# Optimization experiments

Measured on AMD Instinct MI355X. Metric: run time of the kernel, lower is better.

## Reference

```python
import jax, jax.numpy as jnp
import numpy as np

B, T, D, H, L = 4, 128, 768, 770, 40  # batch, token_num, bert dim, head hidden, n_labels


def setup_inputs() -> dict:
    key = jax.random.key(0)
    ks = jax.random.split(key, 7)
    hidden = jax.random.normal(ks[0], (B, T + 1, D), dtype=jnp.float32)
    pred_spans = jnp.sort(jax.random.randint(ks[1], (B, 2), 0, T), axis=1)
    span_avail = jax.random.randint(ks[2], (T, T), 0, 2).astype(jnp.int32)
    # torch nn.Linear: weight init N(0, 0.02), bias init N(0, 1) (normal_(bias, 0) -> mean=0, std=1)
    W1 = (jax.random.normal(ks[3], (2 * D + 1, H)) * 0.02).astype(jnp.float32)
    b1 = jax.random.normal(ks[4], (H,), dtype=jnp.float32)
    W2 = (jax.random.normal(ks[5], (H, L)) * 0.02).astype(jnp.float32)
    b2 = jax.random.normal(ks[6], (L,), dtype=jnp.float32)
    return {"hidden": hidden, "W1": W1, "b1": b1, "W2": W2, "b2": b2,
            "pred_spans": pred_spans, "span_avail": span_avail, "token_num": T}


def reference(hidden, W1, b1, W2, b2, pred_spans, span_avail, token_num):
    # vecs[i] = hidden[:, i+1, :]  (skip [CLS])
    vecs = hidden[:, 1:token_num + 1, :]                      # [B, T, D]
    Bv, Tv, Dv = vecs.shape
    starts = pred_spans[:, 0][:, None, None]                  # [B,1,1]
    ends = pred_spans[:, 1][:, None, None]
    ii = jnp.arange(Tv)[:, None]                              # [T,1]
    jj = jnp.arange(Tv)[None, :]                              # [1,T]
    # indication: 2 if (i,j) == pred span; 1 if strictly inside span with i<=j; else 0
    is_full = (ii == starts) & (jj == ends)                   # [B,T,T]
    inside = (starts <= ii) & (ii <= jj) & (jj <= ends) & (~is_full)
    ind = (2 * is_full + inside).astype(hidden.dtype)         # [B,T,T]
    fi = jnp.broadcast_to(vecs[:, :, None, :], (Bv, Tv, Tv, Dv))
    fj = jnp.broadcast_to(vecs[:, None, :, :], (Bv, Tv, Tv, Dv))
    feat = jnp.concatenate([fi, fj, ind[..., None]], axis=-1)  # [B,T,T,2D+1]
    h = jax.nn.relu(feat @ W1 + b1)                            # [B,T,T,H]
    out = h @ W2 + b2                                          # [B,T,T,L]
    # unavailable spans contribute a zeros row (original appends `zeros`)
    mask = (span_avail >= 1)[None, :, :, None]
    out = jnp.where(mask, out, jnp.zeros((), out.dtype))
    out = out.reshape(Bv, Tv * Tv, -1)                         # span index c = i*T + j
    return jax.nn.log_softmax(out, axis=1)
```

## Files before the change

### kernel.cpp

```cpp
#include <hip/hip_runtime.h>
#include <math.h>

#define BB 4
#define TT 128
#define DD 768
#define HD 770
#define HP 800
#define LL 40
#define TP1 129

typedef __attribute__((ext_vector_type(8))) short s16x8;
typedef __attribute__((ext_vector_type(4))) float f32x4;

#define P_OFF   0
#define Q_OFF   409600
#define W2F_OFF 819200
#define BF1_OFF 838400
#define ACC_OFF 1440512

__device__ __forceinline__ unsigned pkbf(float a, float b) {
    unsigned ua = __float_as_uint(a);
    unsigned ub = __float_as_uint(b);
    return ((ua + 0x8000u) >> 16) | ((ub + 0x8000u) & 0xffff0000u);
}
__device__ __forceinline__ unsigned rne1(float v) {
    unsigned x = __float_as_uint(v);
    return (x + 0x7fffu + ((x >> 16) & 1u)) >> 16;
}

__global__ __launch_bounds__(256) void kPrep(const float* __restrict__ W1,
                                             const float* __restrict__ W2,
                                             float* __restrict__ Q,
                                             unsigned* __restrict__ W2f,
                                             unsigned* __restrict__ Bf1,
                                             float* __restrict__ accum) {
    const int bx = blockIdx.x;
    const int tid = threadIdx.x;
    if (bx < 19) {
        int u = bx * 256 + tid;
        if (u >= 4800) return;
        int nt = u / 1600;
        int rem = u - nt * 1600;
        int ks = rem >> 6;
        int lane = rem & 63;
        int kbase = ks * 32 + ((lane >> 4) << 3);
        int l = nt * 16 + (lane & 15);
        unsigned pk[4];
        #pragma unroll
        for (int sp = 0; sp < 4; ++sp) {
            unsigned w[2];
            #pragma unroll
            for (int e = 0; e < 2; ++e) {
                int k = kbase + 2 * sp + e;
                float v = (k < HD && l < LL) ? W2[k * LL + l] : 0.0f;
                w[e] = rne1(v);
            }
            pk[sp] = w[0] | (w[1] << 16);
        }
        ((uint4*)W2f)[u] = make_uint4(pk[0], pk[1], pk[2], pk[3]);
    } else if (bx < 607) {
        int u = (bx - 19) * 256 + tid;
        int lane = u & 63;
        int g = u >> 6;
        int ks = g % 24;
        int g2 = g / 24;
        int nt = g2 % 49;
        int half = g2 / 49;
        int kbase = ks * 32 + ((lane >> 4) << 3);
        int h = nt * 16 + (lane & 15);
        int row0 = half * DD + kbase;
        unsigned pk[4];
        #pragma unroll
        for (int sp = 0; sp < 4; ++sp) {
            unsigned w[2];
            #pragma unroll
            for (int e = 0; e < 2; ++e) {
                float v = (h < HD) ? W1[(size_t)(row0 + 2 * sp + e) * HD + h] : 0.0f;
                w[e] = rne1(v);
            }
            pk[sp] = w[0] | (w[1] << 16);
        }
        ((uint4*)Bf1)[u] = make_uint4(pk[0], pk[1], pk[2], pk[3]);
    } else {
        int u = (bx - 607) * 256 + tid;
        if (u < 160) accum[u] = 0.0f;
        int u2 = u - 160;
        if (u2 >= 0 && u2 < 512 * 30) {
            int row = u2 / 30;
            int h = HD + (u2 - row * 30);
            Q[(size_t)row * HP + h] = 0.0f;
        }
    }
}

__global__ __launch_bounds__(256) void kA(const float* __restrict__ hidden,
                                          const unsigned* __restrict__ Bf1,
                                          const float* __restrict__ b1,
                                          float* __restrict__ P,
                                          float* __restrict__ Q) {
    __shared__ float part[2 * 64 * 8];
    const int tid  = threadIdx.x;
    const int wave = tid >> 6;
    const int lane = tid & 63;
    const int pairl = wave >> 1;
    const int kh    = wave & 1;
    const int pair  = blockIdx.x * 2 + pairl;
    const int mband = pair & 31;
    const int nt    = pair >> 5;
    const int b  = mband >> 3;
    const int tt = mband & 7;
    const int col  = lane & 15;
    const int quad = lane >> 4;

    const float* __restrict__ Arow =
        hidden + (size_t)(b * TP1 + 1 + tt * 16 + col) * DD + (quad << 3);
    const uint4* __restrict__ B0 = (const uint4*)Bf1 + ((size_t)nt * 24) * 64 + lane;
    const uint4* __restrict__ B1 = (const uint4*)Bf1 + ((size_t)(49 + nt) * 24) * 64 + lane;

    f32x4 a0 = (f32x4){0.f, 0.f, 0.f, 0.f};
    f32x4 a1 = (f32x4){0.f, 0.f, 0.f, 0.f};

    const int ks0 = kh * 12;
    #pragma unroll 4
    for (int s = 0; s < 12; ++s) {
        const int ks = ks0 + s;
        float4 x0 = *(const float4*)(Arow + ks * 32);
        float4 x1 = *(const float4*)(Arow + ks * 32 + 4);
        union { unsigned u[4]; s16x8 v; } af;
        af.u[0] = pkbf(x0.x, x0.y); af.u[1] = pkbf(x0.z, x0.w);
        af.u[2] = pkbf(x1.x, x1.y); af.u[3] = pkbf(x1.z, x1.w);
        union { uint4 q; s16x8 v; } bf0, bf1;
        bf0.q = B0[ks * 64];
        bf1.q = B1[ks * 64];
        a0 = __builtin_amdgcn_mfma_f32_16x16x32_bf16(af.v, bf0.v, a0, 0, 0, 0);
        a1 = __builtin_amdgcn_mfma_f32_16x16x32_bf16(af.v, bf1.v, a1, 0, 0, 0);
    }

    if (kh == 1) {
        float* dst = part + (pairl * 64 + lane) * 8;
        dst[0] = a0[0]; dst[1] = a0[1]; dst[2] = a0[2]; dst[3] = a0[3];
        dst[4] = a1[0]; dst[5] = a1[1]; dst[6] = a1[2]; dst[7] = a1[3];
    }
    __syncthreads();
    if (kh == 0) {
        const float* src = part + (pairl * 64 + lane) * 8;
        const int h = nt * 16 + col;
        if (h < HD) {
            const float bv = b1[h];
            #pragma unroll
            for (int r = 0; r < 4; ++r) {
                int t = tt * 16 + quad * 4 + r;
                size_t row = (size_t)(b * TT + t) * HP;
                P[row + h] = a0[r] + src[r] + bv;
                Q[row + h] = a1[r] + src[4 + r];
            }
        }
    }
}

__global__ __launch_bounds__(256) void kB(const float* __restrict__ P,
                                          const float* __restrict__ Q,
                                          const float* __restrict__ W1,
                                          const unsigned* __restrict__ W2f,
                                          const float* __restrict__ b2,
                                          const int* __restrict__ spans,
                                          const int* __restrict__ avail,
                                          float* __restrict__ out,
                                          float* __restrict__ accum) {
    __shared__ unsigned Sb[2][128 * 20];
    __shared__ float var[3 * HP];
    __shared__ int avi[TT];
    __shared__ float sred[192];

    const int i = blockIdx.x;
    const int b = blockIdx.y;
    const int tid = threadIdx.x;
    const int wave = tid >> 6;
    const int lane = tid & 63;

    const int start = spans[b * 2];
    const int end   = spans[b * 2 + 1];

    const int jS = tid >> 1;
    const int hh = (tid & 1) << 4;
    int indS;
    {
        bool isfull = (i == start) && (jS == end);
        bool inside = (start <= i) && (i <= jS) && (jS <= end) && !isfull;
        indS = isfull ? 2 : (inside ? 1 : 0);
    }

    {
        const float* Pi  = P + (size_t)(b * TT + i) * HP;
        const float* w1L = W1 + (size_t)2 * DD * HD;
        for (int h = tid; h < HP; h += 256) {
            float pv = (h < HD) ? Pi[h] : 0.0f;
            float wv = (h < HD) ? w1L[h] : 0.0f;
            var[h]        = pv;
            var[HP + h]   = pv + wv;
            var[2*HP + h] = pv + wv + wv;
        }
        if (tid < TT) avi[tid] = avail[i * TT + tid];
    }
    __syncthreads();

    const float* Qj = Q + (size_t)(b * TT + jS) * HP;
    const float* vb = var + indS * HP;

    auto form = [&](int c, int p) {
        const int h0 = c * 32 + hh;
        const float4* qp = (const float4*)(Qj + h0);
        float4 q0 = qp[0], q1 = qp[1], q2 = qp[2], q3 = qp[3];
        const float4* vp = (const float4*)(vb + h0);
        float4 v0 = vp[0], v1 = vp[1], v2 = vp[2], v3 = vp[3];
        float s0 = fmaxf(v0.x + q0.x, 0.f), s1 = fmaxf(v0.y + q0.y, 0.f);
        float s2 = fmaxf(v0.z + q0.z, 0.f), s3 = fmaxf(v0.w + q0.w, 0.f);
        float s4 = fmaxf(v1.x + q1.x, 0.f), s5 = fmaxf(v1.y + q1.y, 0.f);
        float s6 = fmaxf(v1.z + q1.z, 0.f), s7 = fmaxf(v1.w + q1.w, 0.f);
        float s8 = fmaxf(v2.x + q2.x, 0.f), s9 = fmaxf(v2.y + q2.y, 0.f);
        float sa = fmaxf(v2.z + q2.z, 0.f), sb_ = fmaxf(v2.w + q2.w, 0.f);
        float sc = fmaxf(v3.x + q3.x, 0.f), sd = fmaxf(v3.y + q3.y, 0.f);
        float se = fmaxf(v3.z + q3.z, 0.f), sf = fmaxf(v3.w + q3.w, 0.f);
        uint4* dst = (uint4*)(&Sb[p][jS * 20 + (hh >> 1)]);
        dst[0] = make_uint4(pkbf(s0,s1), pkbf(s2,s3), pkbf(s4,s5), pkbf(s6,s7));
        dst[1] = make_uint4(pkbf(s8,s9), pkbf(sa,sb_), pkbf(sc,sd), pkbf(se,sf));
    };

    f32x4 acc[2][3];
    #pragma unroll
    for (int mt = 0; mt < 2; ++mt)
        #pragma unroll
        for (int nt = 0; nt < 3; ++nt)
            acc[mt][nt] = (f32x4){0.f, 0.f, 0.f, 0.f};

    form(0, 0);
    __syncthreads();

    const int arow0 = (wave * 32 + (lane & 15)) * 20 + ((lane >> 4) << 2);
    for (int c = 0; c < 25; ++c) {
        const int p = c & 1;
        s16x8 bf0 = *(const s16x8*)((const unsigned*)W2f + (( 0 + c) * 64 + lane) * 4);
        s16x8 bf1 = *(const s16x8*)((const unsigned*)W2f + ((25 + c) * 64 + lane) * 4);
        s16x8 bf2 = *(const s16x8*)((const unsigned*)W2f + ((50 + c) * 64 + lane) * 4);
        s16x8 af0 = *(const s16x8*)(&Sb[p][arow0]);
        s16x8 af1 = *(const s16x8*)(&Sb[p][arow0 + 16 * 20]);
        if (c + 1 < 25) form(c + 1, p ^ 1);
        acc[0][0] = __builtin_amdgcn_mfma_f32_16x16x32_bf16(af0, bf0, acc[0][0], 0, 0, 0);
        acc[0][1] = __builtin_amdgcn_mfma_f32_16x16x32_bf16(af0, bf1, acc[0][1], 0, 0, 0);
        acc[0][2] = __builtin_amdgcn_mfma_f32_16x16x32_bf16(af0, bf2, acc[0][2], 0, 0, 0);
        acc[1][0] = __builtin_amdgcn_mfma_f32_16x16x32_bf16(af1, bf0, acc[1][0], 0, 0, 0);
        acc[1][1] = __builtin_amdgcn_mfma_f32_16x16x32_bf16(af1, bf1, acc[1][1], 0, 0, 0);
        acc[1][2] = __builtin_amdgcn_mfma_f32_16x16x32_bf16(af1, bf2, acc[1][2], 0, 0, 0);
        __syncthreads();
    }

    float bias[3];
    #pragma unroll
    for (int nt = 0; nt < 3; ++nt) {
        int l = nt * 16 + (lane & 15);
        bias[nt] = (l < LL) ? b2[l] : 0.0f;
    }
    const int jr0 = wave * 32 + ((lane >> 4) << 2);
    float sE[3] = {0.f, 0.f, 0.f};
    #pragma unroll
    for (int mt = 0; mt < 2; ++mt) {
        #pragma unroll
        for (int r = 0; r < 4; ++r) {
            int j = jr0 + mt * 16 + r;
            bool msk = avi[j] >= 1;
            size_t rowoff = ((size_t)(b * (TT * TT) + i * TT + j)) * LL;
            #pragma unroll
            for (int nt = 0; nt < 3; ++nt) {
                int l = nt * 16 + (lane & 15);
                if (l < LL) {
                    float val = msk ? (acc[mt][nt][r] + bias[nt]) : 0.0f;
                    out[rowoff + l] = val;
                    sE[nt] += __expf(val);
                }
            }
        }
    }
    #pragma unroll
    for (int nt = 0; nt < 3; ++nt) {
        float v = sE[nt];
        v += __shfl_xor(v, 16);
        v += __shfl_xor(v, 32);
        if (lane < 16) sred[wave * 48 + nt * 16 + lane] = v;
    }
    __syncthreads();
    if (tid < 48) {
        float t4 = sred[tid] + sred[48 + tid] + sred[96 + tid] + sred[144 + tid];
        if (tid < LL) atomicAdd(&accum[b * LL + tid], t4);
    }
}

__global__ __launch_bounds__(256) void kD(float* __restrict__ out,
                                          const float* __restrict__ accum) {
    const int idx = blockIdx.x * 256 + threadIdx.x;
    const int e = idx * 4;
    const int b = e / (TT * TT * LL);
    const int l = e % LL;
    float4 v = ((float4*)out)[idx];
    const float* ac = accum + b * LL + l;
    v.x -= __logf(ac[0]); v.y -= __logf(ac[1]);
    v.z -= __logf(ac[2]); v.w -= __logf(ac[3]);
    ((float4*)out)[idx] = v;
}

extern "C" void kernel_launch(void* const* d_in, const int* in_sizes, int n_in,
                              void* d_out, int out_size, void* d_ws, size_t ws_size,
                              hipStream_t stream) {
    const float* hidden = (const float*)d_in[0];
    const float* W1     = (const float*)d_in[1];
    const float* b1     = (const float*)d_in[2];
    const float* W2     = (const float*)d_in[3];
    const float* b2     = (const float*)d_in[4];
    const int*   spans  = (const int*)d_in[5];
    const int*   avail  = (const int*)d_in[6];
    float* out = (float*)d_out;
    float* ws  = (float*)d_ws;

    float*    P     = ws + P_OFF;
    float*    Q     = ws + Q_OFF;
    unsigned* W2f   = (unsigned*)(ws + W2F_OFF);
    unsigned* Bf1   = (unsigned*)(ws + BF1_OFF);
    float*    accum = ws + ACC_OFF;

    kPrep<<<dim3(668),    dim3(256), 0, stream>>>(W1, W2, Q, W2f, Bf1, accum);
    kA   <<<dim3(784),    dim3(256), 0, stream>>>(hidden, Bf1, b1, P, Q);
    kB   <<<dim3(TT, BB), dim3(256), 0, stream>>>(P, Q, W1, W2f, b2, spans, avail, out, accum);
    kD   <<<dim3(2560),   dim3(256), 0, stream>>>(out, accum);
}
```

Baseline: 127.4 us.

## Fuse W1 bf16 repacking into the projection kernel via shared memory

Removes the separate prep kernel and Bf1 workspace. Each projection block now converts its own 16-column W1 slice to bf16 MFMA layout in LDS before running the full K loop, and the split-K reduction through shared memory is dropped. The W2 packing, accumulator zeroing and Q padding zeroing move into extra blocks of the same launch. This saves a kernel launch and a global write/read of the packed weights, but W1 is now re-read and re-converted by 8 blocks per column tile, and there are fewer waves per output.

Measured after the change: 125.4 us. About the same (-1.6%).

```diff
diff --git a/kernel.cpp b/kernel.cpp
--- a/kernel.cpp
+++ b/kernel.cpp
@@ -15,8 +15,7 @@
 #define P_OFF   0
 #define Q_OFF   409600
 #define W2F_OFF 819200
-#define BF1_OFF 838400
-#define ACC_OFF 1440512
+#define ACC_OFF 838400
 
 __device__ __forceinline__ unsigned pkbf(float a, float b) {
     unsigned ua = __float_as_uint(a);
@@ -28,23 +27,92 @@
     return (x + 0x7fffu + ((x >> 16) & 1u)) >> 16;
 }
 
-__global__ __launch_bounds__(256) void kPrep(const float* __restrict__ W1,
-                                             const float* __restrict__ W2,
-                                             float* __restrict__ Q,
-                                             unsigned* __restrict__ W2f,
-                                             unsigned* __restrict__ Bf1,
-                                             float* __restrict__ accum) {
-    const int bx = blockIdx.x;
+__global__ __launch_bounds__(256) void kA(const float* __restrict__ hidden,
+                                          const float* __restrict__ W1,
+                                          const float* __restrict__ W2,
+                                          const float* __restrict__ b1,
+                                          float* __restrict__ P,
+                                          float* __restrict__ Q,
+                                          unsigned* __restrict__ W2f,
+                                          float* __restrict__ accum) {
+    __shared__ uint4 Bl[3072];
+    const int bx  = blockIdx.x;
     const int tid = threadIdx.x;
-    if (bx < 19) {
-        int u = bx * 256 + tid;
+
+    if (bx < 392) {
+        const int nt = bx / 8;
+        const int mg = bx - nt * 8;
+        const int lane = tid & 63;
+        const int col  = lane & 15;
+        const int quad = lane >> 4;
+
+        for (int u = tid; u < 3072; u += 256) {
+            int half = u / 1536;
+            int rem  = u - half * 1536;
+            int ks = rem >> 6;
+            int ln = rem & 63;
+            int kbase = ks * 32 + ((ln >> 4) << 3);
+            int h = nt * 16 + (ln & 15);
+            int row0 = half * DD + kbase;
+            unsigned pk[4];
+            #pragma unroll
+            for (int sp = 0; sp < 4; ++sp) {
+                unsigned w[2];
+                #pragma unroll
+                for (int e = 0; e < 2; ++e) {
+                    float v = (h < HD) ? W1[(size_t)(row0 + 2 * sp + e) * HD + h] : 0.0f;
+                    w[e] = rne1(v);
+                }
+                pk[sp] = w[0] | (w[1] << 16);
+            }
+            Bl[u] = make_uint4(pk[0], pk[1], pk[2], pk[3]);
+        }
+        __syncthreads();
+
+        const int mband = mg * 4 + (tid >> 6);
+        const int b  = mband >> 3;
+        const int tt = mband & 7;
+
+        const float* __restrict__ Arow =
+            hidden + (size_t)(b * TP1 + 1 + tt * 16 + col) * DD + (quad << 3);
+
+        f32x4 a0 = (f32x4){0.f, 0.f, 0.f, 0.f};
+        f32x4 a1 = (f32x4){0.f, 0.f, 0.f, 0.f};
+
+        #pragma unroll 4
+        for (int ks = 0; ks < 24; ++ks) {
+            float4 x0 = *(const float4*)(Arow + ks * 32);
+            float4 x1 = *(const float4*)(Arow + ks * 32 + 4);
+            union { unsigned u[4]; s16x8 v; } af;
+            af.u[0] = pkbf(x0.x, x0.y); af.u[1] = pkbf(x0.z, x0.w);
+            af.u[2] = pkbf(x1.x, x1.y); af.u[3] = pkbf(x1.z, x1.w);
+            union { uint4 q; s16x8 v; } bf0, bf1;
+            bf0.q = Bl[ks * 64 + lane];
+            bf1.q = Bl[1536 + ks * 64 + lane];
+            a0 = __builtin_amdgcn_mfma_f32_16x16x32_bf16(af.v, bf0.v, a0, 0, 0, 0);
+            a1 = __builtin_amdgcn_mfma_f32_16x16x32_bf16(af.v, bf1.v, a1, 0, 0, 0);
+        }
+
+        const int h = nt * 16 + col;
+        if (h < HD) {
+            const float bv = b1[h];
+            #pragma unroll
+            for (int r = 0; r < 4; ++r) {
+                int t = tt * 16 + quad * 4 + r;
+                size_t row = (size_t)(b * TT + t) * HP;
+                P[row + h] = a0[r] + bv;
+                Q[row + h] = a1[r];
+            }
+        }
+    } else if (bx < 411) {
+        int u = (bx - 392) * 256 + tid;
         if (u >= 4800) return;
         int nt = u / 1600;
         int rem = u - nt * 1600;
         int ks = rem >> 6;
-        int lane = rem & 63;
-        int kbase = ks * 32 + ((lane >> 4) << 3);
-        int l = nt * 16 + (lane & 15);
+        int ln = rem & 63;
+        int kbase = ks * 32 + ((ln >> 4) << 3);
+        int l = nt * 16 + (ln & 15);
         unsigned pk[4];
         #pragma unroll
         for (int sp = 0; sp < 4; ++sp) {
@@ -58,103 +126,13 @@
             pk[sp] = w[0] | (w[1] << 16);
         }
         ((uint4*)W2f)[u] = make_uint4(pk[0], pk[1], pk[2], pk[3]);
-    } else if (bx < 607) {
-        int u = (bx - 19) * 256 + tid;
-        int lane = u & 63;
-        int g = u >> 6;
-        int ks = g % 24;
-        int g2 = g / 24;
-        int nt = g2 % 49;
-        int half = g2 / 49;
-        int kbase = ks * 32 + ((lane >> 4) << 3);
-        int h = nt * 16 + (lane & 15);
-        int row0 = half * DD + kbase;
-        unsigned pk[4];
-        #pragma unroll
-        for (int sp = 0; sp < 4; ++sp) {
-            unsigned w[2];
-            #pragma unroll
-            for (int e = 0; e < 2; ++e) {
-                float v = (h < HD) ? W1[(size_t)(row0 + 2 * sp + e) * HD + h] : 0.0f;
-                w[e] = rne1(v);
-            }
-            pk[sp] = w[0] | (w[1] << 16);
-        }
-        ((uint4*)Bf1)[u] = make_uint4(pk[0], pk[1], pk[2], pk[3]);
+    } else if (bx == 411) {
+        if (tid < 160) accum[tid] = 0.0f;
     } else {
-        int u = (bx - 607) * 256 + tid;
-        if (u < 160) accum[u] = 0.0f;
-        int u2 = u - 160;
-        if (u2 >= 0 && u2 < 512 * 30) {
-            int row = u2 / 30;
-            int h = HD + (u2 - row * 30);
-            Q[(size_t)row * HP + h] = 0.0f;
-        }
-    }
-}
-
-__global__ __launch_bounds__(256) void kA(const float* __restrict__ hidden,
-                                          const unsigned* __restrict__ Bf1,
-                                          const float* __restrict__ b1,
-                                          float* __restrict__ P,
-                                          float* __restrict__ Q) {
-    __shared__ float part[2 * 64 * 8];
-    const int tid  = threadIdx.x;
-    const int wave = tid >> 6;
-    const int lane = tid & 63;
-    const int pairl = wave >> 1;
-    const int kh    = wave & 1;
-    const int pair  = blockIdx.x * 2 + pairl;
-    const int mband = pair & 31;
-    const int nt    = pair >> 5;
-    const int b  = mband >> 3;
-    const int tt = mband & 7;
-    const int col  = lane & 15;
-    const int quad = lane >> 4;
-
-    const float* __restrict__ Arow =
-        hidden + (size_t)(b * TP1 + 1 + tt * 16 + col) * DD + (quad << 3);
-    const uint4* __restrict__ B0 = (const uint4*)Bf1 + ((size_t)nt * 24) * 64 + lane;
-    const uint4* __restrict__ B1 = (const uint4*)Bf1 + ((size_t)(49 + nt) * 24) * 64 + lane;
-
-    f32x4 a0 = (f32x4){0.f, 0.f, 0.f, 0.f};
-    f32x4 a1 = (f32x4){0.f, 0.f, 0.f, 0.f};
-
-    const int ks0 = kh * 12;
-    #pragma unroll 4
-    for (int s = 0; s < 12; ++s) {
-        const int ks = ks0 + s;
-        float4 x0 = *(const float4*)(Arow + ks * 32);
-        float4 x1 = *(const float4*)(Arow + ks * 32 + 4);
-        union { unsigned u[4]; s16x8 v; } af;
-        af.u[0] = pkbf(x0.x, x0.y); af.u[1] = pkbf(x0.z, x0.w);
-        af.u[2] = pkbf(x1.x, x1.y); af.u[3] = pkbf(x1.z, x1.w);
-        union { uint4 q; s16x8 v; } bf0, bf1;
-        bf0.q = B0[ks * 64];
-        bf1.q = B1[ks * 64];
-        a0 = __builtin_amdgcn_mfma_f32_16x16x32_bf16(af.v, bf0.v, a0, 0, 0, 0);
-        a1 = __builtin_amdgcn_mfma_f32_16x16x32_bf16(af.v, bf1.v, a1, 0, 0, 0);
-    }
-
-    if (kh == 1) {
-        float* dst = part + (pairl * 64 + lane) * 8;
-        dst[0] = a0[0]; dst[1] = a0[1]; dst[2] = a0[2]; dst[3] = a0[3];
-        dst[4] = a1[0]; dst[5] = a1[1]; dst[6] = a1[2]; dst[7] = a1[3];
-    }
-    __syncthreads();
-    if (kh == 0) {
-        const float* src = part + (pairl * 64 + lane) * 8;
-        const int h = nt * 16 + col;
-        if (h < HD) {
-            const float bv = b1[h];
-            #pragma unroll
-            for (int r = 0; r < 4; ++r) {
-                int t = tt * 16 + quad * 4 + r;
-                size_t row = (size_t)(b * TT + t) * HP;
-                P[row + h] = a0[r] + src[r] + bv;
-                Q[row + h] = a1[r] + src[4 + r];
-            }
-        }
+        int u = (bx - 412) * 256 + tid;
+        int row = u / 30;
+        int h = HD + (u - row * 30);
+        Q[(size_t)row * HP + h] = 0.0f;
     }
 }
 
@@ -323,11 +301,9 @@
     float*    P     = ws + P_OFF;
     float*    Q     = ws + Q_OFF;
     unsigned* W2f   = (unsigned*)(ws + W2F_OFF);
-    unsigned* Bf1   = (unsigned*)(ws + BF1_OFF);
     float*    accum = ws + ACC_OFF;
 
-    kPrep<<<dim3(668),    dim3(256), 0, stream>>>(W1, W2, Q, W2f, Bf1, accum);
-    kA   <<<dim3(784),    dim3(256), 0, stream>>>(hidden, Bf1, b1, P, Q);
-    kB   <<<dim3(TT, BB), dim3(256), 0, stream>>>(P, Q, W1, W2f, b2, spans, avail, out, accum);
-    kD   <<<dim3(2560),   dim3(256), 0, stream>>>(out, accum);
-}
+    kA <<<dim3(472),    dim3(256), 0, stream>>>(hidden, W1, W2, b1, P, Q, W2f, accum);
+    kB <<<dim3(TT, BB), dim3(256), 0, stream>>>(P, Q, W1, W2f, b2, spans, avail, out, accum);
+    kD <<<dim3(2560),   dim3(256), 0, stream>>>(out, accum);
+}
```
